# Kernel optimization log

Measured on AMD Instinct MI355X. Metric: run time of the kernel, lower is better.

The kernel has to match this reference:

```python
import jax, jax.numpy as jnp
import numpy as np

HEADS = 8
DIM_HEAD = 64
QLEVEL = 127.0  # symmetric int8: clamp to [-128, 127]


def fake_quant(x):
    """Symmetric per-tensor int8 fake quantization with straight-through estimator."""
    delta = jnp.max(jnp.abs(x)) / QLEVEL
    xq = jnp.clip(jnp.round(x / delta), -128.0, 127.0) * delta
    return x + jax.lax.stop_gradient(xq - x)


def setup_inputs() -> dict:
    key = jax.random.key(0)
    ks = jax.random.split(key, 7)
    b, n, m, d, dc = 2, 4096, 1024, 512, 768
    return {
        "x": jax.random.normal(ks[0], (b, n, d), jnp.float32),
        "context": jax.random.normal(ks[1], (b, m, dc), jnp.float32),
        "Wq": jax.random.normal(ks[2], (d, d), jnp.float32) * 0.02,
        "Wk": jax.random.normal(ks[3], (dc, d), jnp.float32) * 0.02,
        "Wv": jax.random.normal(ks[4], (dc, d), jnp.float32) * 0.02,
        "Wo": jax.random.normal(ks[5], (d, d), jnp.float32) * 0.02,
        "bo": jnp.zeros((d,), jnp.float32),
    }


def reference(x, context, Wq, Wk, Wv, Wo, bo):
    b, n, _ = x.shape
    h, dh = HEADS, DIM_HEAD
    scale = dh ** -0.5

    q = x @ Wq            # [b, n, h*dh]
    k = context @ Wk      # [b, m, h*dh]
    v = context @ Wv      # [b, m, h*dh]

    def split(t):  # b n (h d) -> b h n d
        return t.reshape(t.shape[0], t.shape[1], h, dh).transpose(0, 2, 1, 3)

    q, k, v = split(q), split(k), split(v)

    # fake-quantize q and k before the score matmul (use_aq=True path)
    q = fake_quant(q)
    k = fake_quant(k)
    sim = jnp.einsum('bhid,bhjd->bhij', q, k) * scale  # [b, h, n, m]
    attn = jax.nn.softmax(sim, axis=-1)

    # fake-quantize attention weights and v before the AV matmul
    out = jnp.einsum('bhij,bhjd->bhid', fake_quant(attn), fake_quant(v))
    out = out.transpose(0, 2, 1, 3).reshape(b, n, h * dh)  # b h n d -> b n (h d)
    return out @ Wo + bo  # to_out[0]; to_out[-1] is Dropout (identity in eval)
```

## Files before the change

### kernel.cpp

```cpp
#include <hip/hip_runtime.h>
#include <stdint.h>

typedef float  v4f  __attribute__((ext_vector_type(4)));
typedef int    v4i  __attribute__((ext_vector_type(4)));
typedef __bf16 v8bf __attribute__((ext_vector_type(8)));
typedef __bf16 v4bf __attribute__((ext_vector_type(4)));

#define BATCH  2
#define NQ     4096
#define MK     1024
#define DMODEL 512
#define DCTX   768
#define NH     8
#define DH     64

__global__ __launch_bounds__(256) void k_prep(
    const float* __restrict__ x, const float* __restrict__ ctx,
    __bf16* __restrict__ xb, __bf16* __restrict__ cb,
    const float* __restrict__ Wq, const float* __restrict__ Wk,
    const float* __restrict__ Wv, const float* __restrict__ Wo,
    __bf16* __restrict__ Wq_t, __bf16* __restrict__ Wk_t,
    __bf16* __restrict__ Wv_t, __bf16* __restrict__ Wo_t,
    unsigned* __restrict__ scal) {
  int bx = blockIdx.x;
  if (bx < 2816) {
    const int XC = BATCH * NQ * DMODEL / 8;
    const int CC = BATCH * MK * DCTX / 8;
    int idx = bx * 256 + threadIdx.x;
    const float* src; __bf16* dst;
    if (idx < XC) { src = x + (size_t)idx * 8; dst = xb + (size_t)idx * 8; }
    else {
      int j = idx - XC;
      if (j >= CC) return;
      src = ctx + (size_t)j * 8; dst = cb + (size_t)j * 8;
    }
    float4 a = *(const float4*)src, b = *(const float4*)(src + 4);
    v8bf o = { (__bf16)a.x, (__bf16)a.y, (__bf16)a.z, (__bf16)a.w,
               (__bf16)b.x, (__bf16)b.y, (__bf16)b.z, (__bf16)b.w };
    *(v8bf*)dst = o;
    return;
  }
  int id = bx - 2816;
  if (id == 0 && threadIdx.x < 4) scal[threadIdx.x] = 0u;
  int tx = id & 15, rem = id >> 4;
  int ty = rem % 24, tz = rem / 24;
  const float* src; __bf16* dst; int K;
  switch (tz) {
    case 0:  src = Wq; dst = Wq_t; K = DMODEL; break;
    case 1:  src = Wk; dst = Wk_t; K = DCTX;   break;
    case 2:  src = Wv; dst = Wv_t; K = DCTX;   break;
    default: src = Wo; dst = Wo_t; K = DMODEL; break;
  }
  int k0 = ty * 32;
  if (k0 >= K) return;
  int n0 = tx * 32;
  __shared__ __bf16 tile[32][33];
  int c = threadIdx.x & 31, r0 = threadIdx.x >> 5;
  for (int i = 0; i < 4; ++i) {
    int r = r0 + i * 8;
    tile[c][r] = (__bf16)src[(size_t)(k0 + r) * DMODEL + n0 + c];
  }
  __syncthreads();
  for (int i = 0; i < 4; ++i) {
    int r = r0 + i * 8;
    dst[(size_t)(n0 + r) * K + k0 + c] = tile[r][c];
  }
}

template<int K_, int NC, bool BIAS, bool AMAX>
__device__ __forceinline__ void gemm_body(
    char* smemraw, const __bf16* __restrict__ A, const __bf16* __restrict__ Bt,
    float* __restrict__ C, int N, int rowBlk, int colBlk,
    const float* __restrict__ bias,
    unsigned* __restrict__ amaxLo, unsigned* __restrict__ amaxHi) {
  constexpr int CS = K_ + 8;
  constexpr int GPC = K_ / 8;
  constexpr int JT = NC / 16;
  constexpr int NIT = K_ / 32;
  constexpr int AD = 4;
  constexpr int AF = 4;
  __bf16* Bs = (__bf16*)smemraw;
  float* redmax = (float*)(smemraw + (size_t)NC * CS * 2);
  const int tid = threadIdx.x;
  const int lane = tid & 63, wave = tid >> 6;
  const int l15 = lane & 15, g = lane >> 4;
  const int col0 = colBlk * NC;
  const int row0w = rowBlk * 256 + wave * 64;

#pragma unroll
  for (int i = 0; i < NC * GPC / 256; ++i) {
    int f = i * 256 + tid;
    int c = f / GPC, w = f - c * GPC;
    *(v8bf*)(&Bs[c * CS + w * 8]) =
        *(const v8bf*)(Bt + (size_t)(col0 + c) * K_ + w * 8);
  }

  const __bf16* ap[AF];
#pragma unroll
  for (int f = 0; f < AF; ++f)
    ap[f] = A + (size_t)(row0w + f * 16 + l15) * K_ + g * 8;

  v8bf abuf[AF][AD];
#pragma unroll
  for (int i = 0; i < AD; ++i)
#pragma unroll
    for (int f = 0; f < AF; ++f)
      abuf[f][i] = *(const v8bf*)(ap[f] + i * 32);
  __syncthreads();

  v8bf bbuf[2][JT];
#pragma unroll
  for (int j = 0; j < JT; ++j)
    bbuf[0][j] = *(const v8bf*)(&Bs[(j * 16 + l15) * CS + g * 8]);

  v4f acc[AF][JT] = {};
#pragma unroll
  for (int it = 0; it < NIT; ++it) {
    const int cur = it & 1, nxt = cur ^ 1;
    if (it + 1 < NIT) {
#pragma unroll
      for (int j = 0; j < JT; ++j)
        bbuf[nxt][j] =
            *(const v8bf*)(&Bs[(j * 16 + l15) * CS + (it + 1) * 32 + g * 8]);
    }
    v8bf af[AF];
#pragma unroll
    for (int f = 0; f < AF; ++f) {
      af[f] = abuf[f][it % AD];
      if (it + AD < NIT)
        abuf[f][it % AD] = *(const v8bf*)(ap[f] + (it + AD) * 32);
    }
#pragma unroll
    for (int f = 0; f < AF; ++f)
#pragma unroll
      for (int j = 0; j < JT; ++j)
        acc[f][j] = __builtin_amdgcn_mfma_f32_16x16x32_bf16(
            af[f], bbuf[cur][j], acc[f][j], 0, 0, 0);
  }

  float lmax = 0.0f;
#pragma unroll
  for (int j = 0; j < JT; ++j) {
    int col = col0 + j * 16 + l15;
    float bv = BIAS ? bias[col] : 0.0f;
#pragma unroll
    for (int f = 0; f < AF; ++f) {
#pragma unroll
      for (int r = 0; r < 4; ++r) {
        int row = row0w + f * 16 + g * 4 + r;
        float cv = acc[f][j][r] + bv;
        C[(size_t)row * N + col] = cv;
        if (AMAX) lmax = fmaxf(lmax, fabsf(cv));
      }
    }
  }
  if (AMAX) {
    for (int off = 32; off > 0; off >>= 1)
      lmax = fmaxf(lmax, __shfl_xor(lmax, off, 64));
    if (lane == 0) redmax[wave] = lmax;
    __syncthreads();
    if (tid == 0) {
      float bm = fmaxf(fmaxf(redmax[0], redmax[1]), fmaxf(redmax[2], redmax[3]));
      atomicMax(col0 < 512 ? amaxLo : amaxHi, __float_as_uint(bm));
    }
  }
}

__global__ __launch_bounds__(256, 2) void k_gemm_qkv(
    const __bf16* __restrict__ xb, const __bf16* __restrict__ Wq_t,
    float* __restrict__ qf,
    const __bf16* __restrict__ cb, const __bf16* __restrict__ Wkv_t,
    float* __restrict__ kvf, unsigned* __restrict__ scal) {
  __shared__ __align__(16) char smem[64 * (512 + 8) * 2 + 16];
  int bid = blockIdx.x;
  if (bid < 256) {
    int xcd = bid & 7, w = bid >> 3;
    gemm_body<512, 64, false, true>(smem, xb, Wq_t, qf, 512,
                                    xcd * 4 + (w >> 3), w & 7, nullptr,
                                    scal + 0, scal + 0);
  } else {
    int id = bid - 256;
    int xcd = id & 7, w = id >> 3;
    gemm_body<768, 32, false, true>(smem, cb, Wkv_t, kvf, 1024,
                                    xcd, w, nullptr,
                                    scal + 1, scal + 2);
  }
}

__global__ __launch_bounds__(256, 2) void k_gemm_out(
    const __bf16* __restrict__ o, const __bf16* __restrict__ Wo_t,
    float* __restrict__ out, const float* __restrict__ bo) {
  __shared__ __align__(16) char smem[64 * (512 + 8) * 2 + 16];
  int xcd = blockIdx.x & 7, w = blockIdx.x >> 3;
  gemm_body<512, 64, true, false>(smem, o, Wo_t, out, 512,
                                  xcd * 4 + (w >> 3), w & 7, bo,
                                  nullptr, nullptr);
}

__global__ __launch_bounds__(256) void k_quant_kv(
    const float* __restrict__ kvf,
    int8_t* __restrict__ k8, int8_t* __restrict__ v8t,
    const unsigned* __restrict__ scal) {
  __shared__ int8_t tile[64][80];
  int bx = blockIdx.x;
  if (bx < 1024) {
    int j = bx * 256 + threadIdx.x;
    int r = j >> 7;
    int c4 = (j & 127) << 2;
    float4 v = *(const float4*)(kvf + (size_t)r * 1024 + c4);
    float s = 127.0f / __uint_as_float(scal[1]);
    int a0 = __float2int_rn(v.x * s), a1 = __float2int_rn(v.y * s);
    int a2 = __float2int_rn(v.z * s), a3 = __float2int_rn(v.w * s);
    a0 = max(-128, min(127, a0)); a1 = max(-128, min(127, a1));
    a2 = max(-128, min(127, a2)); a3 = max(-128, min(127, a3));
    unsigned p = (unsigned)(a0 & 255) | ((unsigned)(a1 & 255) << 8) |
                 ((unsigned)(a2 & 255) << 16) | ((unsigned)(a3 & 255) << 24);
    *(unsigned*)(k8 + (size_t)j * 4) = p;
    return;
  }
  int id = bx - 1024;
  int bh = id >> 4, b = bh >> 3, h = bh & 7;
  int j0 = (id & 15) * 64;
  const float s = 127.0f / __uint_as_float(scal[2]);
  int t = threadIdx.x;
  int j = t >> 2, dh0 = (t & 3) << 4;
  const float* src = kvf + (size_t)(b * MK + j0 + j) * 1024 + 512 + h * DH + dh0;
#pragma unroll
  for (int i = 0; i < 16; i += 4) {
    float4 v = *(const float4*)(src + i);
    int a0 = __float2int_rn(v.x * s), a1 = __float2int_rn(v.y * s);
    int a2 = __float2int_rn(v.z * s), a3 = __float2int_rn(v.w * s);
    tile[dh0 + i + 0][j] = (int8_t)max(-128, min(127, a0));
    tile[dh0 + i + 1][j] = (int8_t)max(-128, min(127, a1));
    tile[dh0 + i + 2][j] = (int8_t)max(-128, min(127, a2));
    tile[dh0 + i + 3][j] = (int8_t)max(-128, min(127, a3));
  }
  __syncthreads();
  int dh = t >> 2, jb = (t & 3) << 4;
  v4i val = *(const v4i*)(&tile[dh][jb]);
  *(v4i*)(v8t + (size_t)(bh * DH + dh) * MK + j0 + jb) = val;
}

__device__ __forceinline__ v4i quant_pack16(const float* p, float s) {
  v4i out;
#pragma unroll
  for (int q = 0; q < 4; ++q) {
    float4 v = *(const float4*)(p + q * 4);
    int a0 = __float2int_rn(v.x * s), a1 = __float2int_rn(v.y * s);
    int a2 = __float2int_rn(v.z * s), a3 = __float2int_rn(v.w * s);
    a0 = max(-128, min(127, a0)); a1 = max(-128, min(127, a1));
    a2 = max(-128, min(127, a2)); a3 = max(-128, min(127, a3));
    out[q] = (int)((unsigned)(a0 & 255) | ((unsigned)(a1 & 255) << 8) |
                   ((unsigned)(a2 & 255) << 16) | ((unsigned)(a3 & 255) << 24));
  }
  return out;
}

__global__ __launch_bounds__(256, 4) void k_pass1(
    const float* __restrict__ qf, int8_t* __restrict__ q8,
    const int8_t* __restrict__ k8,
    float* __restrict__ invz, unsigned* __restrict__ scal) {
  __shared__ __align__(16) int8_t kbuf[2][128 * 72];
  __shared__ float mared[4];
  int bh = blockIdx.y, b = bh >> 3, h = bh & 7;
  int wave = threadIdx.x >> 6, lane = threadIdx.x & 63;
  int l15 = lane & 15, g = lane >> 4;
  int row0 = blockIdx.x * 64;
  int myrow = row0 + wave * 16 + l15;
  const float aq = __uint_as_float(scal[0]), ak = __uint_as_float(scal[1]);
  const float alpha2 = (aq * ak) * (0.125f / (127.0f * 127.0f)) * 1.44269504f;
  const float sq = 127.0f / aq;
  const v4i z4 = {0, 0, 0, 0};
  size_t qoff = (size_t)(b * NQ + myrow) * DMODEL + h * DH + g * 16;
  v4i qfrag = quant_pack16(qf + qoff, sq);
  *(v4i*)(q8 + qoff) = qfrag;
  const int8_t* kbase = k8 + (size_t)b * MK * DMODEL + h * DH;
  const int rs = threadIdx.x >> 2, qs = (threadIdx.x & 3) * 16;
  const int8_t* kls = kbase + (size_t)rs * DMODEL + qs;

  v4i kp0 = *(const v4i*)(kls);
  v4i kp1 = *(const v4i*)(kls + (size_t)64 * DMODEL);
  *(v4i*)(&kbuf[0][rs * 72 + qs]) = kp0;
  *(v4i*)(&kbuf[0][(rs + 64) * 72 + qs]) = kp1;

  float z[4] = {0.f, 0.f, 0.f, 0.f};
  int mi = -(1 << 30);
  for (int tile = 0; tile < 8; ++tile) {
    const int cur = tile & 1;
    __syncthreads();
    if (tile < 7) {
      kp0 = *(const v4i*)(kls + (size_t)((tile + 1) * 128) * DMODEL);
      kp1 = *(const v4i*)(kls + (size_t)((tile + 1) * 128 + 64) * DMODEL);
    }
    float zt = z[tile >> 1];
#pragma unroll
    for (int t = 0; t < 8; ++t) {
      v4i kfrag = *(const v4i*)(&kbuf[cur][(t * 16 + l15) * 72 + g * 16]);
      v4i sa = __builtin_amdgcn_mfma_i32_16x16x64_i8(kfrag, qfrag, z4, 0, 0, 0);
      mi = max(mi, max(max(sa[0], sa[1]), max(sa[2], sa[3])));
      float e0 = __builtin_amdgcn_exp2f((float)sa[0] * alpha2);
      float e1 = __builtin_amdgcn_exp2f((float)sa[1] * alpha2);
      float e2 = __builtin_amdgcn_exp2f((float)sa[2] * alpha2);
      float e3 = __builtin_amdgcn_exp2f((float)sa[3] * alpha2);
      zt += (e0 + e1) + (e2 + e3);
    }
    z[tile >> 1] = zt;
    if (tile < 7) {
      *(v4i*)(&kbuf[cur ^ 1][rs * 72 + qs]) = kp0;
      *(v4i*)(&kbuf[cur ^ 1][(rs + 64) * 72 + qs]) = kp1;
    }
  }
#pragma unroll
  for (int i = 0; i < 4; ++i) {
    z[i] += __shfl_xor(z[i], 16, 64);
    z[i] += __shfl_xor(z[i], 32, 64);
  }
  mi = max(mi, __shfl_xor(mi, 16, 64));
  mi = max(mi, __shfl_xor(mi, 32, 64));
  float zt = (z[0] + z[1]) + (z[2] + z[3]);
  float iz = 1.0f / zt;
  if (g == 0) invz[(size_t)bh * NQ + myrow] = iz;
  float ma = __builtin_amdgcn_exp2f((float)mi * alpha2) * iz;
#pragma unroll
  for (int off = 1; off < 16; off <<= 1)
    ma = fmaxf(ma, __shfl_xor(ma, off, 64));
  if (lane == 0) mared[wave] = ma;
  __syncthreads();
  if (threadIdx.x == 0)
    atomicMax(scal + 3,
              __float_as_uint(fmaxf(fmaxf(mared[0], mared[1]),
                                    fmaxf(mared[2], mared[3]))));
}

__global__ __launch_bounds__(256, 4) void k_pass2(
    const int8_t* __restrict__ q8, const int8_t* __restrict__ k8,
    const int8_t* __restrict__ v8t, const float* __restrict__ invz,
    const unsigned* __restrict__ scal, __bf16* __restrict__ o) {
  __shared__ __align__(16) int8_t kbuf[2][128 * 72];
  __shared__ __align__(16) int8_t vbuf[2][64 * 152];
  int bh = blockIdx.y, b = bh >> 3, h = bh & 7;
  int wave = threadIdx.x >> 6, lane = threadIdx.x & 63;
  int l15 = lane & 15, g = lane >> 4;
  int row0 = blockIdx.x * 64;
  int myrow = row0 + wave * 16 + l15;
  const float aq = __uint_as_float(scal[0]), ak = __uint_as_float(scal[1]);
  const float avv = __uint_as_float(scal[2]), izm = __uint_as_float(scal[3]);
  const float alpha2 = (aq * ak) * (0.125f / (127.0f * 127.0f)) * 1.44269504f;
  const float oscale = (izm / 127.0f) * (avv / 127.0f);
  const float MAGIC = 12582912.0f;
  const v4i z4 = {0, 0, 0, 0};

  v4i qfrag = *(const v4i*)(q8 + (size_t)(b * NQ + myrow) * DMODEL + h * DH + g * 16);
  const float lcr = __builtin_amdgcn_logf(invz[(size_t)bh * NQ + myrow] * (127.0f / izm));
  const int8_t* kbase = k8 + (size_t)b * MK * DMODEL + h * DH;
  const int8_t* vbase = v8t + (size_t)bh * DH * MK;
  const int rs = threadIdx.x >> 2, qs = (threadIdx.x & 3) * 16;
  const int vr = threadIdx.x >> 3, vq = (threadIdx.x & 7) * 16;
  const int8_t* kls = kbase + (size_t)rs * DMODEL + qs;
  const int8_t* vls = vbase + (size_t)vr * MK + vq;

  v4i kp0 = *(const v4i*)(kls);
  v4i kp1 = *(const v4i*)(kls + (size_t)64 * DMODEL);
  v4i vp0 = *(const v4i*)(vls);
  v4i vp1 = *(const v4i*)(vls + (size_t)32 * MK);
  *(v4i*)(&kbuf[0][rs * 72 + qs]) = kp0;
  *(v4i*)(&kbuf[0][(rs + 64) * 72 + qs]) = kp1;
  *(v4i*)(&vbuf[0][vr * 152 + vq]) = vp0;
  *(v4i*)(&vbuf[0][(vr + 32) * 152 + vq]) = vp1;

  v4i pacc[4] = {};
  for (int tile = 0; tile < 8; ++tile) {
    const int cur = tile & 1;
    __syncthreads();
    if (tile < 7) {
      kp0 = *(const v4i*)(kls + (size_t)((tile + 1) * 128) * DMODEL);
      kp1 = *(const v4i*)(kls + (size_t)((tile + 1) * 128 + 64) * DMODEL);
      vp0 = *(const v4i*)(vls + (tile + 1) * 128);
      vp1 = *(const v4i*)(vls + (size_t)32 * MK + (tile + 1) * 128);
    }
    int w[8];
#pragma unroll
    for (int t = 0; t < 8; ++t) {
      v4i kfrag = *(const v4i*)(&kbuf[cur][(t * 16 + l15) * 72 + g * 16]);
      v4i sa = __builtin_amdgcn_mfma_i32_16x16x64_i8(kfrag, qfrag, z4, 0, 0, 0);
      float f0 = __builtin_amdgcn_exp2f(fmaf((float)sa[0], alpha2, lcr)) + MAGIC;
      float f1 = __builtin_amdgcn_exp2f(fmaf((float)sa[1], alpha2, lcr)) + MAGIC;
      float f2 = __builtin_amdgcn_exp2f(fmaf((float)sa[2], alpha2, lcr)) + MAGIC;
      float f3 = __builtin_amdgcn_exp2f(fmaf((float)sa[3], alpha2, lcr)) + MAGIC;
      w[t] = (int)((__float_as_uint(f0) & 255u) |
                   ((__float_as_uint(f1) & 255u) << 8) |
                   ((__float_as_uint(f2) & 255u) << 16) |
                   (__float_as_uint(f3) << 24));
    }
#pragma unroll
    for (int c = 0; c < 2; ++c) {
      int wc0 = w[c * 4 + 0], wc1 = w[c * 4 + 1];
      int wc2 = w[c * 4 + 2], wc3 = w[c * 4 + 3];
      int t0 = (g & 1) ? wc0 : wc1;
      int r0 = __shfl_xor(t0, 16, 64);
      int t1 = (g & 1) ? wc2 : wc3;
      int r1 = __shfl_xor(t1, 16, 64);
      int a0 = (g & 1) ? r0 : wc0;
      int a1 = (g & 1) ? wc1 : r0;
      int a2 = (g & 1) ? r1 : wc2;
      int a3 = (g & 1) ? wc3 : r1;
      int u0 = (g & 2) ? a0 : a2;
      int s0 = __shfl_xor(u0, 32, 64);
      int u1 = (g & 2) ? a1 : a3;
      int s1 = __shfl_xor(u1, 32, 64);
      v4i afrag;
      afrag[0] = (g & 2) ? s0 : a0;
      afrag[1] = (g & 2) ? s1 : a1;
      afrag[2] = (g & 2) ? a2 : s0;
      afrag[3] = (g & 2) ? a3 : s1;
#pragma unroll
      for (int d = 0; d < 4; ++d) {
        v4i vfrag = *(const v4i*)(&vbuf[cur][(d * 16 + l15) * 152 + c * 64 + g * 16]);
        pacc[d] = __builtin_amdgcn_mfma_i32_16x16x64_i8(vfrag, afrag, pacc[d], 0, 0, 0);
      }
    }
    if (tile < 7) {
      *(v4i*)(&kbuf[cur ^ 1][rs * 72 + qs]) = kp0;
      *(v4i*)(&kbuf[cur ^ 1][(rs + 64) * 72 + qs]) = kp1;
      *(v4i*)(&vbuf[cur ^ 1][vr * 152 + vq]) = vp0;
      *(v4i*)(&vbuf[cur ^ 1][(vr + 32) * 152 + vq]) = vp1;
    }
  }
  __bf16* obase = o + (size_t)(b * NQ + row0 + wave * 16 + l15) * DMODEL + h * DH;
#pragma unroll
  for (int d = 0; d < 4; ++d) {
    v4bf ov;
#pragma unroll
    for (int r = 0; r < 4; ++r)
      ov[r] = (__bf16)((float)pacc[d][r] * oscale);
    *(v4bf*)(obase + d * 16 + g * 4) = ov;
  }
}

extern "C" void kernel_launch(void* const* d_in, const int* in_sizes, int n_in,
                              void* d_out, int out_size, void* d_ws, size_t ws_size,
                              hipStream_t stream) {
  (void)in_sizes; (void)n_in; (void)out_size; (void)ws_size;
  const float* x   = (const float*)d_in[0];
  const float* ctx = (const float*)d_in[1];
  const float* Wq  = (const float*)d_in[2];
  const float* Wk  = (const float*)d_in[3];
  const float* Wv  = (const float*)d_in[4];
  const float* Wo  = (const float*)d_in[5];
  const float* bo  = (const float*)d_in[6];
  float* out = (float*)d_out;

  char* ws = (char*)d_ws;
  size_t off = 0;
  auto alloc = [&](size_t bytes) {
    char* p = ws + off;
    off += (bytes + 255) & ~(size_t)255;
    return p;
  };
  unsigned* scal = (unsigned*)alloc(16);
  __bf16* Wq_t = (__bf16*)alloc((size_t)512 * 512 * 2);
  __bf16* Wk_t = (__bf16*)alloc((size_t)512 * 768 * 2);
  __bf16* Wv_t = (__bf16*)alloc((size_t)512 * 768 * 2);
  __bf16* Wo_t = (__bf16*)alloc((size_t)512 * 512 * 2);
  __bf16* xb   = (__bf16*)alloc((size_t)BATCH * NQ * DMODEL * 2);
  __bf16* cb   = (__bf16*)alloc((size_t)BATCH * MK * DCTX * 2);
  float* qf  = (float*)alloc((size_t)BATCH * NQ * DMODEL * 4);
  float* kvf = (float*)alloc((size_t)BATCH * MK * 1024 * 4);
  int8_t* q8 = (int8_t*)alloc((size_t)BATCH * NQ * DMODEL);
  int8_t* k8 = (int8_t*)alloc((size_t)BATCH * MK * DMODEL);
  int8_t* v8t = (int8_t*)alloc((size_t)BATCH * NH * DH * MK);
  float* invz = (float*)alloc((size_t)BATCH * NH * NQ * 4);
  __bf16* o = (__bf16*)qf;

  k_prep<<<4352, 256, 0, stream>>>(x, ctx, xb, cb, Wq, Wk, Wv, Wo,
                                   Wq_t, Wk_t, Wv_t, Wo_t, scal);
  k_gemm_qkv<<<512, 256, 0, stream>>>(xb, Wq_t, qf, cb, Wk_t, kvf, scal);
  k_quant_kv<<<1280, 256, 0, stream>>>(kvf, k8, v8t, scal);
  k_pass1<<<dim3(64, 16), 256, 0, stream>>>(qf, q8, k8, invz, scal);
  k_pass2<<<dim3(64, 16), 256, 0, stream>>>(q8, k8, v8t, invz, scal, o);
  k_gemm_out<<<256, 256, 0, stream>>>(o, Wo_t, out, bo);
}
```

Baseline: 170.2 us.

## Fuse attention passes into one cooperative kernel with grid-wide sync

Merges the two attention passes into a single cooperative kernel. Each block keeps its quantized Q fragment and row normalizer in registers across a grid.sync that publishes the global attention max, so q8 and invz no longer go through global memory and one launch is saved. The V tile is prefetched before the sync. Cooperative launch needs all 1024 blocks resident at once, and the grid barrier adds a stall, so the original two-kernel path is kept as a fallback if the launch fails.

Measured after the change: 310.6 us. +82.5%, slower.

```diff
diff --git a/kernel.cpp b/kernel.cpp
--- a/kernel.cpp
+++ b/kernel.cpp
@@ -1,4 +1,5 @@
 #include <hip/hip_runtime.h>
+#include <hip/hip_cooperative_groups.h>
 #include <stdint.h>
 
 typedef float  v4f  __attribute__((ext_vector_type(4)));
@@ -254,6 +255,171 @@
                    ((unsigned)(a2 & 255) << 16) | ((unsigned)(a3 & 255) << 24));
   }
   return out;
+}
+
+__global__ __launch_bounds__(256, 4) void k_pass12(
+    const float* __restrict__ qf, const int8_t* __restrict__ k8,
+    const int8_t* __restrict__ v8t, unsigned* __restrict__ scal,
+    __bf16* __restrict__ o) {
+  __shared__ __align__(16) int8_t kbuf[2][128 * 72];
+  __shared__ __align__(16) int8_t vbuf[2][64 * 152];
+  __shared__ float mared[4];
+  int bh = blockIdx.y, b = bh >> 3, h = bh & 7;
+  int wave = threadIdx.x >> 6, lane = threadIdx.x & 63;
+  int l15 = lane & 15, g = lane >> 4;
+  int row0 = blockIdx.x * 64;
+  int myrow = row0 + wave * 16 + l15;
+  const float aq = __uint_as_float(scal[0]), ak = __uint_as_float(scal[1]);
+  const float avv = __uint_as_float(scal[2]);
+  const float alpha2 = (aq * ak) * (0.125f / (127.0f * 127.0f)) * 1.44269504f;
+  const float sq = 127.0f / aq;
+  const float MAGIC = 12582912.0f;
+  const v4i z4 = {0, 0, 0, 0};
+
+  size_t qoff = (size_t)(b * NQ + myrow) * DMODEL + h * DH + g * 16;
+  v4i qfrag = quant_pack16(qf + qoff, sq);
+  const int8_t* kbase = k8 + (size_t)b * MK * DMODEL + h * DH;
+  const int8_t* vbase = v8t + (size_t)bh * DH * MK;
+  const int rs = threadIdx.x >> 2, qs = (threadIdx.x & 3) * 16;
+  const int vr = threadIdx.x >> 3, vq = (threadIdx.x & 7) * 16;
+  const int8_t* kls = kbase + (size_t)rs * DMODEL + qs;
+  const int8_t* vls = vbase + (size_t)vr * MK + vq;
+
+  v4i kp0 = *(const v4i*)(kls);
+  v4i kp1 = *(const v4i*)(kls + (size_t)64 * DMODEL);
+  *(v4i*)(&kbuf[0][rs * 72 + qs]) = kp0;
+  *(v4i*)(&kbuf[0][(rs + 64) * 72 + qs]) = kp1;
+
+  float z[4] = {0.f, 0.f, 0.f, 0.f};
+  int mi = -(1 << 30);
+  for (int tile = 0; tile < 8; ++tile) {
+    const int cur = tile & 1;
+    __syncthreads();
+    if (tile < 7) {
+      kp0 = *(const v4i*)(kls + (size_t)((tile + 1) * 128) * DMODEL);
+      kp1 = *(const v4i*)(kls + (size_t)((tile + 1) * 128 + 64) * DMODEL);
+    }
+    float zt = z[tile >> 1];
+#pragma unroll
+    for (int t = 0; t < 8; ++t) {
+      v4i kfrag = *(const v4i*)(&kbuf[cur][(t * 16 + l15) * 72 + g * 16]);
+      v4i sa = __builtin_amdgcn_mfma_i32_16x16x64_i8(kfrag, qfrag, z4, 0, 0, 0);
+      mi = max(mi, max(max(sa[0], sa[1]), max(sa[2], sa[3])));
+      float e0 = __builtin_amdgcn_exp2f((float)sa[0] * alpha2);
+      float e1 = __builtin_amdgcn_exp2f((float)sa[1] * alpha2);
+      float e2 = __builtin_amdgcn_exp2f((float)sa[2] * alpha2);
+      float e3 = __builtin_amdgcn_exp2f((float)sa[3] * alpha2);
+      zt += (e0 + e1) + (e2 + e3);
+    }
+    z[tile >> 1] = zt;
+    if (tile < 7) {
+      *(v4i*)(&kbuf[cur ^ 1][rs * 72 + qs]) = kp0;
+      *(v4i*)(&kbuf[cur ^ 1][(rs + 64) * 72 + qs]) = kp1;
+    }
+  }
+#pragma unroll
+  for (int i = 0; i < 4; ++i) {
+    z[i] += __shfl_xor(z[i], 16, 64);
+    z[i] += __shfl_xor(z[i], 32, 64);
+  }
+  mi = max(mi, __shfl_xor(mi, 16, 64));
+  mi = max(mi, __shfl_xor(mi, 32, 64));
+  float zt = (z[0] + z[1]) + (z[2] + z[3]);
+  float iz = 1.0f / zt;
+  float ma = __builtin_amdgcn_exp2f((float)mi * alpha2) * iz;
+#pragma unroll
+  for (int off = 1; off < 16; off <<= 1)
+    ma = fmaxf(ma, __shfl_xor(ma, off, 64));
+
+  v4i vp0 = *(const v4i*)(vls);
+  v4i vp1 = *(const v4i*)(vls + (size_t)32 * MK);
+  *(v4i*)(&vbuf[0][vr * 152 + vq]) = vp0;
+  *(v4i*)(&vbuf[0][(vr + 32) * 152 + vq]) = vp1;
+
+  if (lane == 0) mared[wave] = ma;
+  __syncthreads();
+  if (threadIdx.x == 0)
+    atomicMax(scal + 3,
+              __float_as_uint(fmaxf(fmaxf(mared[0], mared[1]),
+                                    fmaxf(mared[2], mared[3]))));
+  cooperative_groups::this_grid().sync();
+
+  const float izm = __uint_as_float(scal[3]);
+  const float oscale = (izm / 127.0f) * (avv / 127.0f);
+  const float lcr = __builtin_amdgcn_logf(iz * (127.0f / izm));
+
+  kp0 = *(const v4i*)(kls);
+  kp1 = *(const v4i*)(kls + (size_t)64 * DMODEL);
+  *(v4i*)(&kbuf[0][rs * 72 + qs]) = kp0;
+  *(v4i*)(&kbuf[0][(rs + 64) * 72 + qs]) = kp1;
+
+  v4i pacc[4] = {};
+  for (int tile = 0; tile < 8; ++tile) {
+    const int cur = tile & 1;
+    __syncthreads();
+    if (tile < 7) {
+      kp0 = *(const v4i*)(kls + (size_t)((tile + 1) * 128) * DMODEL);
+      kp1 = *(const v4i*)(kls + (size_t)((tile + 1) * 128 + 64) * DMODEL);
+      vp0 = *(const v4i*)(vls + (tile + 1) * 128);
+      vp1 = *(const v4i*)(vls + (size_t)32 * MK + (tile + 1) * 128);
+    }
+    int w[8];
+#pragma unroll
+    for (int t = 0; t < 8; ++t) {
+      v4i kfrag = *(const v4i*)(&kbuf[cur][(t * 16 + l15) * 72 + g * 16]);
+      v4i sa = __builtin_amdgcn_mfma_i32_16x16x64_i8(kfrag, qfrag, z4, 0, 0, 0);
+      float f0 = __builtin_amdgcn_exp2f(fmaf((float)sa[0], alpha2, lcr)) + MAGIC;
+      float f1 = __builtin_amdgcn_exp2f(fmaf((float)sa[1], alpha2, lcr)) + MAGIC;
+      float f2 = __builtin_amdgcn_exp2f(fmaf((float)sa[2], alpha2, lcr)) + MAGIC;
+      float f3 = __builtin_amdgcn_exp2f(fmaf((float)sa[3], alpha2, lcr)) + MAGIC;
+      w[t] = (int)((__float_as_uint(f0) & 255u) |
+                   ((__float_as_uint(f1) & 255u) << 8) |
+                   ((__float_as_uint(f2) & 255u) << 16) |
+                   (__float_as_uint(f3) << 24));
+    }
+#pragma unroll
+    for (int c = 0; c < 2; ++c) {
+      int wc0 = w[c * 4 + 0], wc1 = w[c * 4 + 1];
+      int wc2 = w[c * 4 + 2], wc3 = w[c * 4 + 3];
+      int t0 = (g & 1) ? wc0 : wc1;
+      int r0 = __shfl_xor(t0, 16, 64);
+      int t1 = (g & 1) ? wc2 : wc3;
+      int r1 = __shfl_xor(t1, 16, 64);
+      int a0 = (g & 1) ? r0 : wc0;
+      int a1 = (g & 1) ? wc1 : r0;
+      int a2 = (g & 1) ? r1 : wc2;
+      int a3 = (g & 1) ? wc3 : r1;
+      int u0 = (g & 2) ? a0 : a2;
+      int s0 = __shfl_xor(u0, 32, 64);
+      int u1 = (g & 2) ? a1 : a3;
+      int s1 = __shfl_xor(u1, 32, 64);
+      v4i afrag;
+      afrag[0] = (g & 2) ? s0 : a0;
+      afrag[1] = (g & 2) ? s1 : a1;
+      afrag[2] = (g & 2) ? a2 : s0;
+      afrag[3] = (g & 2) ? a3 : s1;
+#pragma unroll
+      for (int d = 0; d < 4; ++d) {
+        v4i vfrag = *(const v4i*)(&vbuf[cur][(d * 16 + l15) * 152 + c * 64 + g * 16]);
+        pacc[d] = __builtin_amdgcn_mfma_i32_16x16x64_i8(vfrag, afrag, pacc[d], 0, 0, 0);
+      }
+    }
+    if (tile < 7) {
+      *(v4i*)(&kbuf[cur ^ 1][rs * 72 + qs]) = kp0;
+      *(v4i*)(&kbuf[cur ^ 1][(rs + 64) * 72 + qs]) = kp1;
+      *(v4i*)(&vbuf[cur ^ 1][vr * 152 + vq]) = vp0;
+      *(v4i*)(&vbuf[cur ^ 1][(vr + 32) * 152 + vq]) = vp1;
+    }
+  }
+  __bf16* obase = o + (size_t)(b * NQ + row0 + wave * 16 + l15) * DMODEL + h * DH;
+#pragma unroll
+  for (int d = 0; d < 4; ++d) {
+    v4bf ov;
+#pragma unroll
+    for (int r = 0; r < 4; ++r)
+      ov[r] = (__bf16)((float)pacc[d][r] * oscale);
+    *(v4bf*)(obase + d * 16 + g * 4) = ov;
+  }
 }
 
 __global__ __launch_bounds__(256, 4) void k_pass1(
@@ -476,7 +642,16 @@
                                    Wq_t, Wk_t, Wv_t, Wo_t, scal);
   k_gemm_qkv<<<512, 256, 0, stream>>>(xb, Wq_t, qf, cb, Wk_t, kvf, scal);
   k_quant_kv<<<1280, 256, 0, stream>>>(kvf, k8, v8t, scal);
-  k_pass1<<<dim3(64, 16), 256, 0, stream>>>(qf, q8, k8, invz, scal);
-  k_pass2<<<dim3(64, 16), 256, 0, stream>>>(q8, k8, v8t, invz, scal, o);
+
+  void* args[] = {(void*)&qf, (void*)&k8, (void*)&v8t, (void*)&scal, (void*)&o};
+  hipError_t ce = hipLaunchCooperativeKernel((const void*)k_pass12,
+                                             dim3(64, 16), dim3(256, 1, 1),
+                                             args, 0, stream);
+  if (ce != hipSuccess) {
+    (void)hipGetLastError();
+    k_pass1<<<dim3(64, 16), 256, 0, stream>>>(qf, q8, k8, invz, scal);
+    k_pass2<<<dim3(64, 16), 256, 0, stream>>>(q8, k8, v8t, invz, scal, o);
+  }
+
   k_gemm_out<<<256, 256, 0, stream>>>(o, Wo_t, out, bo);
 }
```

## Load K/V MFMA fragments directly from global memory instead of LDS staging

Applied to the files above, without the earlier changes.

Both attention passes drop the double-buffered shared-memory staging of K and V tiles. Each lane now reads its int8 MFMA fragments straight from global memory, relying on L1/L2 caching because all waves share the same K/V. This removes LDS traffic, per-tile __syncthreads barriers and the register prefetch. In exchange every wave issues its own global loads, which raises cache and memory traffic and may expose load latency that the prefetch used to hide.

Measured after the change: 223.8 us. 1.31x slower.

```diff
diff --git a/kernel.cpp b/kernel.cpp
--- a/kernel.cpp
+++ b/kernel.cpp
@@ -260,7 +260,6 @@
     const float* __restrict__ qf, int8_t* __restrict__ q8,
     const int8_t* __restrict__ k8,
     float* __restrict__ invz, unsigned* __restrict__ scal) {
-  __shared__ __align__(16) int8_t kbuf[2][128 * 72];
   __shared__ float mared[4];
   int bh = blockIdx.y, b = bh >> 3, h = bh & 7;
   int wave = threadIdx.x >> 6, lane = threadIdx.x & 63;
@@ -274,28 +273,16 @@
   size_t qoff = (size_t)(b * NQ + myrow) * DMODEL + h * DH + g * 16;
   v4i qfrag = quant_pack16(qf + qoff, sq);
   *(v4i*)(q8 + qoff) = qfrag;
-  const int8_t* kbase = k8 + (size_t)b * MK * DMODEL + h * DH;
-  const int rs = threadIdx.x >> 2, qs = (threadIdx.x & 3) * 16;
-  const int8_t* kls = kbase + (size_t)rs * DMODEL + qs;
-
-  v4i kp0 = *(const v4i*)(kls);
-  v4i kp1 = *(const v4i*)(kls + (size_t)64 * DMODEL);
-  *(v4i*)(&kbuf[0][rs * 72 + qs]) = kp0;
-  *(v4i*)(&kbuf[0][(rs + 64) * 72 + qs]) = kp1;
+  const int8_t* kf0 = k8 + (size_t)b * MK * DMODEL + h * DH +
+                      (size_t)l15 * DMODEL + g * 16;
 
   float z[4] = {0.f, 0.f, 0.f, 0.f};
   int mi = -(1 << 30);
   for (int tile = 0; tile < 8; ++tile) {
-    const int cur = tile & 1;
-    __syncthreads();
-    if (tile < 7) {
-      kp0 = *(const v4i*)(kls + (size_t)((tile + 1) * 128) * DMODEL);
-      kp1 = *(const v4i*)(kls + (size_t)((tile + 1) * 128 + 64) * DMODEL);
-    }
     float zt = z[tile >> 1];
 #pragma unroll
     for (int t = 0; t < 8; ++t) {
-      v4i kfrag = *(const v4i*)(&kbuf[cur][(t * 16 + l15) * 72 + g * 16]);
+      v4i kfrag = *(const v4i*)(kf0 + (size_t)(tile * 128 + t * 16) * DMODEL);
       v4i sa = __builtin_amdgcn_mfma_i32_16x16x64_i8(kfrag, qfrag, z4, 0, 0, 0);
       mi = max(mi, max(max(sa[0], sa[1]), max(sa[2], sa[3])));
       float e0 = __builtin_amdgcn_exp2f((float)sa[0] * alpha2);
@@ -305,10 +292,6 @@
       zt += (e0 + e1) + (e2 + e3);
     }
     z[tile >> 1] = zt;
-    if (tile < 7) {
-      *(v4i*)(&kbuf[cur ^ 1][rs * 72 + qs]) = kp0;
-      *(v4i*)(&kbuf[cur ^ 1][(rs + 64) * 72 + qs]) = kp1;
-    }
   }
 #pragma unroll
   for (int i = 0; i < 4; ++i) {
@@ -336,8 +319,6 @@
     const int8_t* __restrict__ q8, const int8_t* __restrict__ k8,
     const int8_t* __restrict__ v8t, const float* __restrict__ invz,
     const unsigned* __restrict__ scal, __bf16* __restrict__ o) {
-  __shared__ __align__(16) int8_t kbuf[2][128 * 72];
-  __shared__ __align__(16) int8_t vbuf[2][64 * 152];
   int bh = blockIdx.y, b = bh >> 3, h = bh & 7;
   int wave = threadIdx.x >> 6, lane = threadIdx.x & 63;
   int l15 = lane & 15, g = lane >> 4;
@@ -352,36 +333,16 @@
 
   v4i qfrag = *(const v4i*)(q8 + (size_t)(b * NQ + myrow) * DMODEL + h * DH + g * 16);
   const float lcr = __builtin_amdgcn_logf(invz[(size_t)bh * NQ + myrow] * (127.0f / izm));
-  const int8_t* kbase = k8 + (size_t)b * MK * DMODEL + h * DH;
-  const int8_t* vbase = v8t + (size_t)bh * DH * MK;
-  const int rs = threadIdx.x >> 2, qs = (threadIdx.x & 3) * 16;
-  const int vr = threadIdx.x >> 3, vq = (threadIdx.x & 7) * 16;
-  const int8_t* kls = kbase + (size_t)rs * DMODEL + qs;
-  const int8_t* vls = vbase + (size_t)vr * MK + vq;
-
-  v4i kp0 = *(const v4i*)(kls);
-  v4i kp1 = *(const v4i*)(kls + (size_t)64 * DMODEL);
-  v4i vp0 = *(const v4i*)(vls);
-  v4i vp1 = *(const v4i*)(vls + (size_t)32 * MK);
-  *(v4i*)(&kbuf[0][rs * 72 + qs]) = kp0;
-  *(v4i*)(&kbuf[0][(rs + 64) * 72 + qs]) = kp1;
-  *(v4i*)(&vbuf[0][vr * 152 + vq]) = vp0;
-  *(v4i*)(&vbuf[0][(vr + 32) * 152 + vq]) = vp1;
+  const int8_t* kf0 = k8 + (size_t)b * MK * DMODEL + h * DH +
+                      (size_t)l15 * DMODEL + g * 16;
+  const int8_t* vf0 = v8t + (size_t)bh * DH * MK + (size_t)l15 * MK + g * 16;
 
   v4i pacc[4] = {};
   for (int tile = 0; tile < 8; ++tile) {
-    const int cur = tile & 1;
-    __syncthreads();
-    if (tile < 7) {
-      kp0 = *(const v4i*)(kls + (size_t)((tile + 1) * 128) * DMODEL);
-      kp1 = *(const v4i*)(kls + (size_t)((tile + 1) * 128 + 64) * DMODEL);
-      vp0 = *(const v4i*)(vls + (tile + 1) * 128);
-      vp1 = *(const v4i*)(vls + (size_t)32 * MK + (tile + 1) * 128);
-    }
     int w[8];
 #pragma unroll
     for (int t = 0; t < 8; ++t) {
-      v4i kfrag = *(const v4i*)(&kbuf[cur][(t * 16 + l15) * 72 + g * 16]);
+      v4i kfrag = *(const v4i*)(kf0 + (size_t)(tile * 128 + t * 16) * DMODEL);
       v4i sa = __builtin_amdgcn_mfma_i32_16x16x64_i8(kfrag, qfrag, z4, 0, 0, 0);
       float f0 = __builtin_amdgcn_exp2f(fmaf((float)sa[0], alpha2, lcr)) + MAGIC;
       float f1 = __builtin_amdgcn_exp2f(fmaf((float)sa[1], alpha2, lcr)) + MAGIC;
@@ -415,15 +376,9 @@
       afrag[3] = (g & 2) ? a3 : s1;
 #pragma unroll
       for (int d = 0; d < 4; ++d) {
-        v4i vfrag = *(const v4i*)(&vbuf[cur][(d * 16 + l15) * 152 + c * 64 + g * 16]);
+        v4i vfrag = *(const v4i*)(vf0 + (size_t)(d * 16) * MK + tile * 128 + c * 64);
         pacc[d] = __builtin_amdgcn_mfma_i32_16x16x64_i8(vfrag, afrag, pacc[d], 0, 0, 0);
       }
-    }
-    if (tile < 7) {
-      *(v4i*)(&kbuf[cur ^ 1][rs * 72 + qs]) = kp0;
-      *(v4i*)(&kbuf[cur ^ 1][(rs + 64) * 72 + qs]) = kp1;
-      *(v4i*)(&vbuf[cur ^ 1][vr * 152 + vq]) = vp0;
-      *(v4i*)(&vbuf[cur ^ 1][(vr + 32) * 152 + vq]) = vp1;
     }
   }
   __bf16* obase = o + (size_t)(b * NQ + row0 + wave * 16 + l15) * DMODEL + h * DH;
```
